# Performance work log

Hardware: AMD Instinct MI355X
Metric: run time of the kernel (lower is better)

## Reference

```python
import jax, jax.numpy as jnp
import numpy as np

V, H, NH, L, NL = 30522, 768, 12, 4, 2  # vocab, hidden, heads, layers, labels
B, S = 4, 1024
HD = H // NH  # head dim = 64


def setup_inputs() -> dict:
    key = jax.random.key(0)
    ks = jax.random.split(key, 16)
    sc = 0.02
    return {
        "input_ids": jax.random.randint(ks[0], (B, S), 0, V),
        "emb": jax.random.normal(ks[1], (V, H), jnp.float32) * sc,
        "Wq": jax.random.normal(ks[2], (L, H, H), jnp.float32) * sc,
        "bq": jnp.zeros((L, H), jnp.float32),
        "Wk": jax.random.normal(ks[3], (L, H, H), jnp.float32) * sc,
        "bk": jnp.zeros((L, H), jnp.float32),
        "Wv": jax.random.normal(ks[4], (L, H, H), jnp.float32) * sc,
        "bv": jnp.zeros((L, H), jnp.float32),
        "Wi": jax.random.normal(ks[5], (L, H, H), jnp.float32) * sc,
        "bi": jnp.zeros((L, H), jnp.float32),
        "Wo": jax.random.normal(ks[6], (L, H, H), jnp.float32) * sc,
        "bo": jnp.zeros((L, H), jnp.float32),
        "Wc": jax.random.normal(ks[7], (NL, H), jnp.float32) * sc,
        "bc": jnp.zeros((NL,), jnp.float32),
    }


def _encoder(x, Wq, bq, Wk, bk, Wv, bv, Wi, bi, Wo, bo):
    def layer(h, p):
        wq, bq_, wk, bk_, wv, bv_, wi, bi_, wo, bo_ = p
        def heads(y):  # [B,S,H] -> [B,NH,S,HD]
            return y.reshape(B, S, NH, HD).transpose(0, 2, 1, 3)
        q = heads(h @ wq.T + bq_)
        k = heads(h @ wk.T + bk_)
        v = heads(h @ wv.T + bv_)
        scores = jnp.einsum("bhqd,bhkd->bhqk", q, k) / jnp.sqrt(jnp.float32(HD))
        probs = jax.nn.softmax(scores, axis=-1)  # dropout is identity (eval)
        ctx = jnp.einsum("bhqk,bhkd->bhqd", probs, v)
        attn_out = ctx.transpose(0, 2, 1, 3).reshape(B, S, H)
        inter = jax.nn.relu(attn_out @ wi.T + bi_)
        out = inter @ wo.T + bo_ + attn_out  # residual adds attention output
        return out, None

    x, _ = jax.lax.scan(layer, x, (Wq, bq, Wk, bk, Wv, bv, Wi, bi, Wo, bo))
    return x


def reference(input_ids, emb, Wq, bq, Wk, bk, Wv, bv, Wi, bi, Wo, bo, Wc, bc):
    x = emb[input_ids]  # [B,S,H]
    x = _encoder(x, Wq, bq, Wk, bk, Wv, bv, Wi, bi, Wo, bo)
    pooled = x[:, 0]  # [B,H]
    logits = pooled @ Wc.T + bc  # [B,NL]
    return logits
```

## Files before the change

### kernel.cpp

```cpp
#include <hip/hip_runtime.h>
#include <hip/hip_bf16.h>
#include <math.h>

constexpr int Hdim = 768;
constexpr int NH   = 12;
constexpr int HD   = 64;
constexpr int NLAYER = 4;
constexpr int Bb   = 4;
constexpr int Ss   = 1024;
constexpr int Mm   = Bb * Ss;
constexpr int NL   = 2;
constexpr int PL   = Bb * NH * Ss;
constexpr float LOG2E = 1.44269504088896f;

typedef _Float16 f16x8 __attribute__((ext_vector_type(8)));
typedef _Float16 f16x4 __attribute__((ext_vector_type(4)));
typedef __fp16   h16x2 __attribute__((ext_vector_type(2)));
typedef float    f32x4 __attribute__((ext_vector_type(4)));

__device__ __forceinline__ f32x4 mfma32h(f16x8 a, f16x8 b, f32x4 c) {
#if __has_builtin(__builtin_amdgcn_mfma_f32_16x16x32_f16)
    return __builtin_amdgcn_mfma_f32_16x16x32_f16(a, b, c, 0, 0, 0);
#else
    asm("v_mfma_f32_16x16x32_f16 %0, %1, %2, %0" : "+v"(c) : "v"(a), "v"(b));
    return c;
#endif
}
__device__ __forceinline__ f32x4 mfma16h(f16x4 a, f16x4 b, f32x4 c) {
#if __has_builtin(__builtin_amdgcn_mfma_f32_16x16x16f16)
    return __builtin_amdgcn_mfma_f32_16x16x16f16(a, b, c, 0, 0, 0);
#else
    asm("v_mfma_f32_16x16x16_f16 %0, %1, %2, %0" : "+v"(c) : "v"(a), "v"(b));
    return c;
#endif
}

__device__ __forceinline__ void gload16(const void* g, void* l) {
    __builtin_amdgcn_global_load_lds(
        (const __attribute__((address_space(1))) unsigned int*)g,
        (__attribute__((address_space(3))) unsigned int*)l, 16, 0, 0);
}

__global__ void prep_kernel(const int* __restrict__ ids,
                            const float* __restrict__ emb,
                            float* __restrict__ x32, _Float16* __restrict__ xh,
                            const float* __restrict__ Wq, const float* __restrict__ Wk,
                            const float* __restrict__ Wv, const float* __restrict__ Wi,
                            const float* __restrict__ Wo,
                            _Float16* __restrict__ w16) {
    if (blockIdx.x < 3072) {
        int gidx = blockIdx.x * 256 + threadIdx.x;
        int row = gidx / 192, t = gidx - row * 192;
        int id = ids[row];
        float4 v = ((const float4*)(emb + (size_t)id * Hdim))[t];
        ((float4*)(x32 + (size_t)row * Hdim))[t] = v;
        f16x4 h;
        h[0] = (_Float16)v.x; h[1] = (_Float16)v.y;
        h[2] = (_Float16)v.z; h[3] = (_Float16)v.w;
        *(f16x4*)(xh + (size_t)row * Hdim + t * 4) = h;
    } else {
        int i = (blockIdx.x - 3072) * 256 + threadIdx.x;
        int l = i / (5 * 147456);
        int rem = i - l * (5 * 147456);
        int which = rem / 147456;
        int j = rem - which * 147456;
        const float* src = (which == 0 ? Wq : which == 1 ? Wk : which == 2 ? Wv
                          : which == 3 ? Wi : Wo) + (size_t)l * 589824;
        float4 v = ((const float4*)src)[j];
        f16x4 h;
        h[0] = (_Float16)v.x; h[1] = (_Float16)v.y;
        h[2] = (_Float16)v.z; h[3] = (_Float16)v.w;
        *(f16x4*)(w16 + ((size_t)l * 5 + which) * 589824 + (size_t)j * 4) = h;
    }
}

template<int BM>
__global__ __launch_bounds__(256) void gemm_f16(
    const _Float16* __restrict__ Xh, const _Float16* __restrict__ Wh,
    const float* __restrict__ b0, const float* __restrict__ b1,
    const float* __restrict__ b2,
    const float* __restrict__ resid32,
    _Float16* __restrict__ Yh, float* __restrict__ Y32,
    int relu, size_t outSeg, float qscale, int gm)
{
    constexpr int ABASE = BM * 64;
    constexpr int NFR   = (BM == 64) ? 4 : 2;
    __shared__ _Float16 lds[ABASE + 8192];

    const int tid = threadIdx.x;
    const int lane = tid & 63, w = tid >> 6;
    const int l15 = lane & 15, g = lane >> 4;

    const int nwg = gridDim.x;
    const int cpx = nwg >> 3;
    const int bid = blockIdx.x;
    const int x   = (bid & 7) * cpx + (bid >> 3);
    const int m0  = (x % gm) * BM;
    const int n0  = (x / gm) * 128;

    const int srow = lane >> 3;
    const int sswz = 8 * ((lane & 7) ^ srow);
    const _Float16* pA;
    _Float16* lA;
    if constexpr (BM == 64) {
        pA = Xh + (size_t)(m0 + w*16 + srow) * Hdim + sswz;
        lA = &lds[0] + w * 1024;
    } else {
        pA = Xh + (size_t)(m0 + w*8 + srow) * Hdim + sswz;
        lA = &lds[0] + w * 512;
    }
    const _Float16* pB = Wh + (size_t)(n0 + w*32 + srow) * Hdim + sswz;
    _Float16* lB = &lds[ABASE] + w * 2048;

    f32x4 acc[2][NFR];
    #pragma unroll
    for (int m = 0; m < 2; ++m)
        #pragma unroll
        for (int n = 0; n < NFR; ++n) acc[m][n] = (f32x4){0.f, 0.f, 0.f, 0.f};

    const int fsw = l15 & 7;

    for (int k0 = 0; k0 < Hdim; k0 += 64) {
        __syncthreads();
        if constexpr (BM == 64) {
            gload16(pA + k0,          lA);
            gload16(pA + k0 + 8*Hdim, lA + 512);
        } else {
            gload16(pA + k0, lA);
        }
        #pragma unroll
        for (int j = 0; j < 4; ++j)
            gload16(pB + k0 + j*8*Hdim, lB + j*512);
        __syncthreads();

        #pragma unroll
        for (int ks = 0; ks < 2; ++ks) {
            const int so = 8 * ((ks*4 + g) ^ fsw);
            f16x8 af[2], bf[NFR];
            #pragma unroll
            for (int m = 0; m < 2; ++m) {
                const int ar = (BM == 64) ? ((w >> 1)*32 + m*16 + l15)
                                          : (m*16 + l15);
                af[m] = *(const f16x8*)&lds[ar * 64 + so];
            }
            #pragma unroll
            for (int n = 0; n < NFR; ++n) {
                const int br = (BM == 64) ? ((w & 1)*64 + n*16 + l15)
                                          : (w*32 + n*16 + l15);
                bf[n] = *(const f16x8*)&lds[ABASE + br * 64 + so];
            }
            #pragma unroll
            for (int m = 0; m < 2; ++m)
                #pragma unroll
                for (int n = 0; n < NFR; ++n)
                    acc[m][n] = mfma32h(af[m], bf[n], acc[m][n]);
        }
    }

    const int rb = (BM == 64) ? (m0 + (w >> 1)*32 + g*4) : (m0 + g*4);
    #pragma unroll
    for (int n = 0; n < NFR; ++n) {
        const int col = (BM == 64) ? (n0 + (w & 1)*64 + n*16 + l15)
                                   : (n0 + w*32 + n*16 + l15);
        const int seg = col / Hdim;
        const int lc  = col - seg * Hdim;
        const float bias = (seg == 0 ? b0 : seg == 1 ? b1 : b2)[lc];
        #pragma unroll
        for (int m = 0; m < 2; ++m) {
            #pragma unroll
            for (int r = 0; r < 4; ++r) {
                const size_t idx = (size_t)seg * outSeg + (size_t)(rb + m*16 + r) * Hdim + lc;
                float v = acc[m][n][r] + bias;
                if (seg == 0) v *= qscale;
                if (relu) v = v > 0.f ? v : 0.f;
                if (resid32) v += resid32[idx];
                Yh[idx] = (_Float16)v;
                if (Y32) Y32[idx] = v;
            }
        }
    }
}

__global__ __launch_bounds__(256, 4) void attn_mfma(
    const _Float16* __restrict__ Qh, const _Float16* __restrict__ Kh,
    const _Float16* __restrict__ Vh,
    float* __restrict__ Op0, float* __restrict__ Op1,
    float* __restrict__ Mp, float* __restrict__ Lp)
{
    __shared__ _Float16 sm[17408];

    const int tid  = threadIdx.x;
    const int lane = tid & 63, wid = tid >> 6;
    const int l15  = lane & 15, g = lane >> 4;
    const int qtile = blockIdx.x >> 1, part = blockIdx.x & 1;
    const int h = blockIdx.y, b = blockIdx.z;

    const size_t rowbase = (size_t)b * Ss;
    const int    colbase = h * HD;
    const int    q0 = qtile * 128 + wid * 32;
    const int    kv0 = part * 512;

    f16x8 qf[2][2];
    #pragma unroll
    for (int nf = 0; nf < 2; ++nf) {
        const size_t r = (rowbase + q0 + nf * 16 + l15) * Hdim + colbase;
        #pragma unroll
        for (int ks = 0; ks < 2; ++ks)
            qf[nf][ks] = *(const f16x8*)(Qh + r + ks * 32 + g * 8);
    }

    f32x4 accO[4][2];
    #pragma unroll
    for (int mf = 0; mf < 4; ++mf)
        #pragma unroll
        for (int nf = 0; nf < 2; ++nf) accO[mf][nf] = (f32x4){0.f, 0.f, 0.f, 0.f};
    float mrun[2] = {-1e30f, -1e30f}, lsum[2] = {0.f, 0.f};

    const int s8 = lane >> 3;
    const int kswz = 8 * ((lane & 7) ^ s8);
    const _Float16* gK = Kh + (rowbase + kv0 + wid*16 + s8) * Hdim + colbase + kswz;

    const int kx = lane ^ (wid << 4);
    const _Float16* gV = Vh + (rowbase + kv0 + lane) * Hdim + colbase + wid * 16;
    uint4 vr[2];

    const int fsw = l15 & 7;

    gload16(gK,          &sm[0] + wid*1024);
    gload16(gK + 8*Hdim, &sm[0] + wid*1024 + 512);
    #pragma unroll
    for (int u = 0; u < 2; ++u) vr[u] = *(const uint4*)(gV + u * 8);
    #pragma unroll
    for (int u = 0; u < 2; ++u) {
        const _Float16* hs = (const _Float16*)&vr[u];
        #pragma unroll
        for (int j = 0; j < 8; ++j)
            sm[8192 + (wid*16 + u*8 + j) * 72 + kx] = hs[j];
    }
    __syncthreads();

    for (int t = 0; t < 8; ++t) {
        const int cur = t & 1;
        const int kb = cur * 4096;
        const int vb = 8192 + cur * 4608;
        if (t < 7) {
            const int nkb = (cur ^ 1) * 4096;
            const size_t ko = (size_t)((t + 1) * 64) * Hdim;
            gload16(gK + ko,          &sm[nkb] + wid*1024);
            gload16(gK + ko + 8*Hdim, &sm[nkb] + wid*1024 + 512);
            #pragma unroll
            for (int u = 0; u < 2; ++u)
                vr[u] = *(const uint4*)(gV + ko + u * 8);
        }

        f32x4 sc[4][2];
        #pragma unroll
        for (int m = 0; m < 4; ++m)
            #pragma unroll
            for (int nf = 0; nf < 2; ++nf) sc[m][nf] = (f32x4){0.f, 0.f, 0.f, 0.f};
        __builtin_amdgcn_s_setprio(1);
        #pragma unroll
        for (int ks = 0; ks < 2; ++ks) {
            const int so = 8 * ((ks*4 + g) ^ fsw);
            #pragma unroll
            for (int m = 0; m < 4; ++m) {
                f16x8 kh_ = *(const f16x8*)&sm[kb + (m * 16 + l15) * 64 + so];
                #pragma unroll
                for (int nf = 0; nf < 2; ++nf)
                    sc[m][nf] = mfma32h(kh_, qf[nf][ks], sc[m][nf]);
            }
        }
        __builtin_amdgcn_s_setprio(0);

        f16x4 pb[4][2];
        #pragma unroll
        for (int nf = 0; nf < 2; ++nf) {
            float tl = -1e30f;
            #pragma unroll
            for (int m = 0; m < 4; ++m)
                #pragma unroll
                for (int r = 0; r < 4; ++r) tl = fmaxf(tl, sc[m][nf][r]);
            if (__any(tl > mrun[nf] + 11.5416f)) {
                float tmax = fmaxf(tl, __shfl_xor(tl, 16));
                tmax = fmaxf(tmax, __shfl_xor(tmax, 32));
                const float mnew = fmaxf(mrun[nf], tmax);
                const float corr = __builtin_amdgcn_exp2f(mrun[nf] - mnew);
                mrun[nf] = mnew;
                lsum[nf] *= corr;
                #pragma unroll
                for (int mf = 0; mf < 4; ++mf) {
                    accO[mf][nf][0] *= corr; accO[mf][nf][1] *= corr;
                    accO[mf][nf][2] *= corr; accO[mf][nf][3] *= corr;
                }
            }
            float ps = 0.f;
            #pragma unroll
            for (int m = 0; m < 4; ++m)
                #pragma unroll
                for (int r = 0; r < 4; ++r) {
                    const float p = __builtin_amdgcn_exp2f(sc[m][nf][r] - mrun[nf]);
                    sc[m][nf][r] = p;
                    ps += p;
                }
            lsum[nf] += ps;
            #pragma unroll
            for (int kt = 0; kt < 4; ++kt) {
                union { h16x2 h2[2]; f16x4 v; } u;
                u.h2[0] = __builtin_amdgcn_cvt_pkrtz(sc[kt][nf][0], sc[kt][nf][1]);
                u.h2[1] = __builtin_amdgcn_cvt_pkrtz(sc[kt][nf][2], sc[kt][nf][3]);
                pb[kt][nf] = u.v;
            }
        }

        if (t < 7) {
            const int nvb = 8192 + (cur ^ 1) * 4608;
            #pragma unroll
            for (int u = 0; u < 2; ++u) {
                const _Float16* hs = (const _Float16*)&vr[u];
                #pragma unroll
                for (int j = 0; j < 8; ++j)
                    sm[nvb + (wid*16 + u*8 + j) * 72 + kx] = hs[j];
            }
        }

        __builtin_amdgcn_s_setprio(1);
        #pragma unroll
        for (int kt = 0; kt < 4; ++kt)
            #pragma unroll
            for (int mf = 0; mf < 4; ++mf) {
                const int voff = vb + (mf * 16 + l15) * 72 + ((kt ^ mf) * 16 + g * 4);
                f16x4 vh_ = *(const f16x4*)&sm[voff];
                #pragma unroll
                for (int nf = 0; nf < 2; ++nf)
                    accO[mf][nf] = mfma16h(vh_, pb[kt][nf], accO[mf][nf]);
            }
        __builtin_amdgcn_s_setprio(0);

        __syncthreads();
    }

    #pragma unroll
    for (int nf = 0; nf < 2; ++nf) {
        lsum[nf] += __shfl_xor(lsum[nf], 16);
        lsum[nf] += __shfl_xor(lsum[nf], 32);
    }
    float* ot = (float*)sm + wid * 2176;
    #pragma unroll
    for (int nf = 0; nf < 2; ++nf) {
        #pragma unroll
        for (int mf = 0; mf < 4; ++mf)
            #pragma unroll
            for (int r = 0; r < 4; ++r)
                ot[(nf * 16 + l15) * 68 + mf * 16 + g * 4 + r] = accO[mf][nf][r];
    }
    if (g == 0) {
        #pragma unroll
        for (int nf = 0; nf < 2; ++nf) {
            const size_t idx = (size_t)part * PL +
                (((size_t)b * NH + h) * Ss + q0 + nf * 16 + l15);
            Mp[idx] = mrun[nf];
            Lp[idx] = lsum[nf];
        }
    }
    __syncthreads();
    float* Op = part ? Op1 : Op0;
    const int orow = lane >> 1, oc = (lane & 1) * 32;
    const size_t pbase = (((size_t)b * NH + h) * Ss + q0 + orow) * 64 + oc;
    #pragma unroll
    for (int i = 0; i < 8; ++i)
        *(float4*)(Op + pbase + i * 4) = *(float4*)&ot[orow * 68 + oc + i * 4];
}

__global__ void merge_kernel(const float* __restrict__ Op0, const float* __restrict__ Op1,
                             const float* __restrict__ Mp, const float* __restrict__ Lp,
                             _Float16* __restrict__ a16, float* __restrict__ a32) {
    const int id = blockIdx.x * 256 + threadIdx.x;
    const int idx = id >> 2, dseg = id & 3;
    const int b = idx / (NH * Ss);
    const int rem = idx - b * NH * Ss;
    const int h = rem / Ss, q = rem - h * Ss;
    const float m0 = Mp[idx], m1 = Mp[PL + idx];
    const float l0 = Lp[idx], l1 = Lp[PL + idx];
    const float M  = fmaxf(m0, m1);
    const float e0 = __builtin_amdgcn_exp2f(m0 - M);
    const float e1 = __builtin_amdgcn_exp2f(m1 - M);
    const float inv = 1.f / (l0 * e0 + l1 * e1);
    const size_t pb = (size_t)idx * 64 + dseg * 16;
    const size_t ga = ((size_t)(b * Ss + q)) * Hdim + h * 64 + dseg * 16;
    #pragma unroll
    for (int i = 0; i < 4; ++i) {
        float4 a = *(const float4*)(Op0 + pb + i * 4);
        float4 c = *(const float4*)(Op1 + pb + i * 4);
        float4 o;
        o.x = (a.x * e0 + c.x * e1) * inv;
        o.y = (a.y * e0 + c.y * e1) * inv;
        o.z = (a.z * e0 + c.z * e1) * inv;
        o.w = (a.w * e0 + c.w * e1) * inv;
        *(float4*)(a32 + ga + i * 4) = o;
        f16x4 hh;
        hh[0] = (_Float16)o.x; hh[1] = (_Float16)o.y;
        hh[2] = (_Float16)o.z; hh[3] = (_Float16)o.w;
        *(f16x4*)(a16 + ga + i * 4) = hh;
    }
}

__global__ void cls_kernel(const float* __restrict__ x32,
                           const float* __restrict__ Wc,
                           const float* __restrict__ bc,
                           float* __restrict__ out) {
    const int b = blockIdx.x >> 1;
    const int n = blockIdx.x & 1;
    const int t = threadIdx.x;
    const float* px = x32 + (size_t)b * Ss * Hdim;
    const float* pw = Wc + (size_t)n * Hdim;
    float partial = 0.f;
    for (int k = t; k < Hdim; k += 256) partial = fmaf(px[k], pw[k], partial);
    __shared__ float red[256];
    red[t] = partial;
    __syncthreads();
    for (int off = 128; off > 0; off >>= 1) {
        if (t < off) red[t] += red[t + off];
        __syncthreads();
    }
    if (t == 0) out[blockIdx.x] = red[0] + bc[n];
}

extern "C" void kernel_launch(void* const* d_in, const int* in_sizes, int n_in,
                              void* d_out, int out_size, void* d_ws, size_t ws_size,
                              hipStream_t stream) {
    const int*   ids = (const int*)d_in[0];
    const float* emb = (const float*)d_in[1];
    const float* Wq  = (const float*)d_in[2];
    const float* bq  = (const float*)d_in[3];
    const float* Wk  = (const float*)d_in[4];
    const float* bk  = (const float*)d_in[5];
    const float* Wv  = (const float*)d_in[6];
    const float* bv  = (const float*)d_in[7];
    const float* Wi  = (const float*)d_in[8];
    const float* bi  = (const float*)d_in[9];
    const float* Wo  = (const float*)d_in[10];
    const float* bo  = (const float*)d_in[11];
    const float* Wc  = (const float*)d_in[12];
    const float* bc  = (const float*)d_in[13];
    float* out = (float*)d_out;

    const size_t F  = (size_t)Mm * Hdim;
    const size_t WS = (size_t)Hdim * Hdim;

    float*    x32 = (float*)d_ws;
    _Float16* xh  = (_Float16*)(x32 + F);
    _Float16* qkv = xh + F;
    _Float16* a16 = qkv + 3 * F;
    _Float16* i16 = a16 + F;
    _Float16* w16 = i16 + F;
    float*    a32 = (float*)(w16 + 20 * WS);
    float*    Op0 = a32 + F;
    float*    Op1 = Op0 + F;
    float*    Mp  = Op1 + F;
    float*    Lp  = Mp + 2 * PL;

    prep_kernel<<<14592, 256, 0, stream>>>(ids, emb, x32, xh, Wq, Wk, Wv, Wi, Wo, w16);

    for (int l = 0; l < NLAYER; ++l) {
        _Float16* wl = w16 + (size_t)l * 5 * WS;
        gemm_f16<64><<<1152, 256, 0, stream>>>(
            xh, wl, bq + l*Hdim, bk + l*Hdim, bv + l*Hdim,
            nullptr, qkv, nullptr, 0, F, 0.125f * LOG2E, 64);
        attn_mfma<<<dim3(16, NH, Bb), 256, 0, stream>>>(
            qkv, qkv + F, qkv + 2*F, Op0, Op1, Mp, Lp);
        merge_kernel<<<PL * 4 / 256, 256, 0, stream>>>(Op0, Op1, Mp, Lp, a16, a32);
        gemm_f16<32><<<768, 256, 0, stream>>>(
            a16, wl + 3*WS, bi + l*Hdim, bi + l*Hdim, bi + l*Hdim,
            nullptr, i16, nullptr, 1, 0, 1.f, 128);
        gemm_f16<32><<<768, 256, 0, stream>>>(
            i16, wl + 4*WS, bo + l*Hdim, bo + l*Hdim, bo + l*Hdim,
            a32, xh, x32, 0, 0, 1.f, 128);
    }

    cls_kernel<<<Bb * NL, 256, 0, stream>>>(x32, Wc, bc, out);
}
```

Measured before the change: 412.6 us.

## Fuse split-attention merge into the Wi GEMM A-load and the Wo GEMM residual epilogue

Drops the separate merge kernel. The intermediate GEMM now combines the two attention partials (Op0/Op1 with their max and sum stats) while loading its A tile, converting to fp16 straight into LDS. The output GEMM recomputes the merged attention value in its epilogue to add as the residual. The fp32 x32 copy is written only on the last layer, which removes the a16/a32 buffers and their traffic, at the cost of redundant stat loads, exp2 and divides in both GEMMs and a loss of async A-tile loads.

```diff
diff --git a/kernel.cpp b/kernel.cpp
--- a/kernel.cpp
+++ b/kernel.cpp
@@ -74,12 +74,13 @@
     }
 }
 
-template<int BM>
+template<int BM, int MODE>
 __global__ __launch_bounds__(256) void gemm_f16(
     const _Float16* __restrict__ Xh, const _Float16* __restrict__ Wh,
     const float* __restrict__ b0, const float* __restrict__ b1,
     const float* __restrict__ b2,
-    const float* __restrict__ resid32,
+    const float* __restrict__ Op0, const float* __restrict__ Op1,
+    const float* __restrict__ Mp, const float* __restrict__ Lp,
     _Float16* __restrict__ Yh, float* __restrict__ Y32,
     int relu, size_t outSeg, float qscale, int gm)
 {
@@ -100,18 +101,21 @@
 
     const int srow = lane >> 3;
     const int sswz = 8 * ((lane & 7) ^ srow);
-    const _Float16* pA;
-    _Float16* lA;
-    if constexpr (BM == 64) {
-        pA = Xh + (size_t)(m0 + w*16 + srow) * Hdim + sswz;
-        lA = &lds[0] + w * 1024;
-    } else {
-        pA = Xh + (size_t)(m0 + w*8 + srow) * Hdim + sswz;
-        lA = &lds[0] + w * 512;
-    }
     const _Float16* pB = Wh + (size_t)(n0 + w*32 + srow) * Hdim + sswz;
     _Float16* lB = &lds[ABASE] + w * 2048;
 
+    const _Float16* pA = nullptr;
+    _Float16* lA = nullptr;
+    if constexpr (MODE != 1) {
+        if constexpr (BM == 64) {
+            pA = Xh + (size_t)(m0 + w*16 + srow) * Hdim + sswz;
+            lA = &lds[0] + w * 1024;
+        } else {
+            pA = Xh + (size_t)(m0 + w*8 + srow) * Hdim + sswz;
+            lA = &lds[0] + w * 512;
+        }
+    }
+
     f32x4 acc[2][NFR];
     #pragma unroll
     for (int m = 0; m < 2; ++m)
@@ -122,11 +126,39 @@
 
     for (int k0 = 0; k0 < Hdim; k0 += 64) {
         __syncthreads();
-        if constexpr (BM == 64) {
-            gload16(pA + k0,          lA);
-            gload16(pA + k0 + 8*Hdim, lA + 512);
+        if constexpr (MODE == 1) {
+            const int r  = tid >> 3;
+            const int sg = tid & 7;
+            const int m  = m0 + r;
+            const size_t idxr = ((size_t)(m >> 10) * NH + (k0 >> 6)) * Ss + (m & 1023);
+            const float m0_ = Mp[idxr], m1_ = Mp[PL + idxr];
+            const float l0_ = Lp[idxr], l1_ = Lp[PL + idxr];
+            const float Mx  = fmaxf(m0_, m1_);
+            const float e0  = __builtin_amdgcn_exp2f(m0_ - Mx);
+            const float e1  = __builtin_amdgcn_exp2f(m1_ - Mx);
+            const float inv = 1.f / (l0_ * e0 + l1_ * e1);
+            const size_t pb2 = idxr * 64 + sg * 8;
+            float4 a0 = *(const float4*)(Op0 + pb2);
+            float4 a1 = *(const float4*)(Op0 + pb2 + 4);
+            float4 c0 = *(const float4*)(Op1 + pb2);
+            float4 c1 = *(const float4*)(Op1 + pb2 + 4);
+            union { h16x2 h2[4]; f16x8 v; } u;
+            u.h2[0] = __builtin_amdgcn_cvt_pkrtz((a0.x*e0 + c0.x*e1)*inv,
+                                                 (a0.y*e0 + c0.y*e1)*inv);
+            u.h2[1] = __builtin_amdgcn_cvt_pkrtz((a0.z*e0 + c0.z*e1)*inv,
+                                                 (a0.w*e0 + c0.w*e1)*inv);
+            u.h2[2] = __builtin_amdgcn_cvt_pkrtz((a1.x*e0 + c1.x*e1)*inv,
+                                                 (a1.y*e0 + c1.y*e1)*inv);
+            u.h2[3] = __builtin_amdgcn_cvt_pkrtz((a1.z*e0 + c1.z*e1)*inv,
+                                                 (a1.w*e0 + c1.w*e1)*inv);
+            *(f16x8*)&lds[r * 64 + 8 * (sg ^ (r & 7))] = u.v;
         } else {
-            gload16(pA + k0, lA);
+            if constexpr (BM == 64) {
+                gload16(pA + k0,          lA);
+                gload16(pA + k0 + 8*Hdim, lA + 512);
+            } else {
+                gload16(pA + k0, lA);
+            }
         }
         #pragma unroll
         for (int j = 0; j < 4; ++j)
@@ -169,11 +201,23 @@
         for (int m = 0; m < 2; ++m) {
             #pragma unroll
             for (int r = 0; r < 4; ++r) {
-                const size_t idx = (size_t)seg * outSeg + (size_t)(rb + m*16 + r) * Hdim + lc;
+                const int row = rb + m*16 + r;
+                const size_t idx = (size_t)seg * outSeg + (size_t)row * Hdim + lc;
                 float v = acc[m][n][r] + bias;
                 if (seg == 0) v *= qscale;
                 if (relu) v = v > 0.f ? v : 0.f;
-                if (resid32) v += resid32[idx];
+                if constexpr (MODE == 2) {
+                    const size_t idxr = ((size_t)(row >> 10) * NH + (lc >> 6)) * Ss
+                                        + (row & 1023);
+                    const float m0_ = Mp[idxr], m1_ = Mp[PL + idxr];
+                    const float l0_ = Lp[idxr], l1_ = Lp[PL + idxr];
+                    const float Mx  = fmaxf(m0_, m1_);
+                    const float e0  = __builtin_amdgcn_exp2f(m0_ - Mx);
+                    const float e1  = __builtin_amdgcn_exp2f(m1_ - Mx);
+                    const float inv = 1.f / (l0_ * e0 + l1_ * e1);
+                    const size_t po = idxr * 64 + (lc & 63);
+                    v += (Op0[po] * e0 + Op1[po] * e1) * inv;
+                }
                 Yh[idx] = (_Float16)v;
                 if (Y32) Y32[idx] = v;
             }
@@ -369,39 +413,6 @@
     #pragma unroll
     for (int i = 0; i < 8; ++i)
         *(float4*)(Op + pbase + i * 4) = *(float4*)&ot[orow * 68 + oc + i * 4];
-}
-
-__global__ void merge_kernel(const float* __restrict__ Op0, const float* __restrict__ Op1,
-                             const float* __restrict__ Mp, const float* __restrict__ Lp,
-                             _Float16* __restrict__ a16, float* __restrict__ a32) {
-    const int id = blockIdx.x * 256 + threadIdx.x;
-    const int idx = id >> 2, dseg = id & 3;
-    const int b = idx / (NH * Ss);
-    const int rem = idx - b * NH * Ss;
-    const int h = rem / Ss, q = rem - h * Ss;
-    const float m0 = Mp[idx], m1 = Mp[PL + idx];
-    const float l0 = Lp[idx], l1 = Lp[PL + idx];
-    const float M  = fmaxf(m0, m1);
-    const float e0 = __builtin_amdgcn_exp2f(m0 - M);
-    const float e1 = __builtin_amdgcn_exp2f(m1 - M);
-    const float inv = 1.f / (l0 * e0 + l1 * e1);
-    const size_t pb = (size_t)idx * 64 + dseg * 16;
-    const size_t ga = ((size_t)(b * Ss + q)) * Hdim + h * 64 + dseg * 16;
-    #pragma unroll
-    for (int i = 0; i < 4; ++i) {
-        float4 a = *(const float4*)(Op0 + pb + i * 4);
-        float4 c = *(const float4*)(Op1 + pb + i * 4);
-        float4 o;
-        o.x = (a.x * e0 + c.x * e1) * inv;
-        o.y = (a.y * e0 + c.y * e1) * inv;
-        o.z = (a.z * e0 + c.z * e1) * inv;
-        o.w = (a.w * e0 + c.w * e1) * inv;
-        *(float4*)(a32 + ga + i * 4) = o;
-        f16x4 hh;
-        hh[0] = (_Float16)o.x; hh[1] = (_Float16)o.y;
-        hh[2] = (_Float16)o.z; hh[3] = (_Float16)o.w;
-        *(f16x4*)(a16 + ga + i * 4) = hh;
-    }
 }
 
 __global__ void cls_kernel(const float* __restrict__ x32,
@@ -450,11 +461,9 @@
     float*    x32 = (float*)d_ws;
     _Float16* xh  = (_Float16*)(x32 + F);
     _Float16* qkv = xh + F;
-    _Float16* a16 = qkv + 3 * F;
-    _Float16* i16 = a16 + F;
+    _Float16* i16 = qkv + 3 * F;
     _Float16* w16 = i16 + F;
-    float*    a32 = (float*)(w16 + 20 * WS);
-    float*    Op0 = a32 + F;
+    float*    Op0 = (float*)(w16 + 20 * WS);
     float*    Op1 = Op0 + F;
     float*    Mp  = Op1 + F;
     float*    Lp  = Mp + 2 * PL;
@@ -463,18 +472,20 @@
 
     for (int l = 0; l < NLAYER; ++l) {
         _Float16* wl = w16 + (size_t)l * 5 * WS;
-        gemm_f16<64><<<1152, 256, 0, stream>>>(
+        gemm_f16<64, 0><<<1152, 256, 0, stream>>>(
             xh, wl, bq + l*Hdim, bk + l*Hdim, bv + l*Hdim,
-            nullptr, qkv, nullptr, 0, F, 0.125f * LOG2E, 64);
+            nullptr, nullptr, nullptr, nullptr,
+            qkv, nullptr, 0, F, 0.125f * LOG2E, 64);
         attn_mfma<<<dim3(16, NH, Bb), 256, 0, stream>>>(
             qkv, qkv + F, qkv + 2*F, Op0, Op1, Mp, Lp);
-        merge_kernel<<<PL * 4 / 256, 256, 0, stream>>>(Op0, Op1, Mp, Lp, a16, a32);
-        gemm_f16<32><<<768, 256, 0, stream>>>(
-            a16, wl + 3*WS, bi + l*Hdim, bi + l*Hdim, bi + l*Hdim,
-            nullptr, i16, nullptr, 1, 0, 1.f, 128);
-        gemm_f16<32><<<768, 256, 0, stream>>>(
+        gemm_f16<32, 1><<<768, 256, 0, stream>>>(
+            nullptr, wl + 3*WS, bi + l*Hdim, bi + l*Hdim, bi + l*Hdim,
+            Op0, Op1, Mp, Lp,
+            i16, nullptr, 1, 0, 1.f, 128);
+        gemm_f16<32, 2><<<768, 256, 0, stream>>>(
             i16, wl + 4*WS, bo + l*Hdim, bo + l*Hdim, bo + l*Hdim,
-            a32, xh, x32, 0, 0, 1.f, 128);
+            Op0, Op1, Mp, Lp,
+            xh, (l == NLAYER - 1) ? x32 : nullptr, 0, 0, 1.f, 128);
     }
 
     cls_kernel<<<Bb * NL, 256, 0, stream>>>(x32, Wc, bc, out);
```

After: 427.5 us. 3.6% more time.

## Store attention partials in fp16 and write fp32 output only for pooled rows

Applied to the files above, without the earlier changes.

The split-KV attention partial outputs are now stored as fp16 instead of fp32, which halves the traffic between the attention and merge kernels. The merge kernel folds the normalisation into per-part scales and uses 8-wide fp16 loads. The fp32 hidden-state copy is no longer written by the embedding prep. The final layer's output GEMM writes fp32 only for the CLS rows that the classifier reads, since the residual uses a32, not x32. The cost is some precision loss in the unnormalised partial outputs stored in fp16.

```diff
diff --git a/kernel.cpp b/kernel.cpp
--- a/kernel.cpp
+++ b/kernel.cpp
@@ -43,7 +43,7 @@
 
 __global__ void prep_kernel(const int* __restrict__ ids,
                             const float* __restrict__ emb,
-                            float* __restrict__ x32, _Float16* __restrict__ xh,
+                            _Float16* __restrict__ xh,
                             const float* __restrict__ Wq, const float* __restrict__ Wk,
                             const float* __restrict__ Wv, const float* __restrict__ Wi,
                             const float* __restrict__ Wo,
@@ -53,7 +53,6 @@
         int row = gidx / 192, t = gidx - row * 192;
         int id = ids[row];
         float4 v = ((const float4*)(emb + (size_t)id * Hdim))[t];
-        ((float4*)(x32 + (size_t)row * Hdim))[t] = v;
         f16x4 h;
         h[0] = (_Float16)v.x; h[1] = (_Float16)v.y;
         h[2] = (_Float16)v.z; h[3] = (_Float16)v.w;
@@ -169,13 +168,14 @@
         for (int m = 0; m < 2; ++m) {
             #pragma unroll
             for (int r = 0; r < 4; ++r) {
-                const size_t idx = (size_t)seg * outSeg + (size_t)(rb + m*16 + r) * Hdim + lc;
+                const int row = rb + m*16 + r;
+                const size_t idx = (size_t)seg * outSeg + (size_t)row * Hdim + lc;
                 float v = acc[m][n][r] + bias;
                 if (seg == 0) v *= qscale;
                 if (relu) v = v > 0.f ? v : 0.f;
                 if (resid32) v += resid32[idx];
                 Yh[idx] = (_Float16)v;
-                if (Y32) Y32[idx] = v;
+                if (Y32 && (row & 1023) == 0) Y32[idx] = v;
             }
         }
     }
@@ -184,7 +184,7 @@
 __global__ __launch_bounds__(256, 4) void attn_mfma(
     const _Float16* __restrict__ Qh, const _Float16* __restrict__ Kh,
     const _Float16* __restrict__ Vh,
-    float* __restrict__ Op0, float* __restrict__ Op1,
+    _Float16* __restrict__ Op0, _Float16* __restrict__ Op1,
     float* __restrict__ Mp, float* __restrict__ Lp)
 {
     __shared__ _Float16 sm[17408];
@@ -344,15 +344,17 @@
         lsum[nf] += __shfl_xor(lsum[nf], 16);
         lsum[nf] += __shfl_xor(lsum[nf], 32);
     }
-    float* ot = (float*)sm + wid * 2176;
-    #pragma unroll
-    for (int nf = 0; nf < 2; ++nf) {
-        #pragma unroll
-        for (int mf = 0; mf < 4; ++mf)
-            #pragma unroll
-            for (int r = 0; r < 4; ++r)
-                ot[(nf * 16 + l15) * 68 + mf * 16 + g * 4 + r] = accO[mf][nf][r];
-    }
+    __syncthreads();
+    _Float16* ot16 = (_Float16*)sm + wid * 2304;
+    #pragma unroll
+    for (int nf = 0; nf < 2; ++nf)
+        #pragma unroll
+        for (int mf = 0; mf < 4; ++mf) {
+            union { h16x2 h2[2]; f16x4 v; } u;
+            u.h2[0] = __builtin_amdgcn_cvt_pkrtz(accO[mf][nf][0], accO[mf][nf][1]);
+            u.h2[1] = __builtin_amdgcn_cvt_pkrtz(accO[mf][nf][2], accO[mf][nf][3]);
+            *(f16x4*)&ot16[(nf * 16 + l15) * 72 + mf * 16 + g * 4] = u.v;
+        }
     if (g == 0) {
         #pragma unroll
         for (int nf = 0; nf < 2; ++nf) {
@@ -363,15 +365,16 @@
         }
     }
     __syncthreads();
-    float* Op = part ? Op1 : Op0;
+    _Float16* Op = part ? Op1 : Op0;
     const int orow = lane >> 1, oc = (lane & 1) * 32;
     const size_t pbase = (((size_t)b * NH + h) * Ss + q0 + orow) * 64 + oc;
     #pragma unroll
-    for (int i = 0; i < 8; ++i)
-        *(float4*)(Op + pbase + i * 4) = *(float4*)&ot[orow * 68 + oc + i * 4];
-}
-
-__global__ void merge_kernel(const float* __restrict__ Op0, const float* __restrict__ Op1,
+    for (int i = 0; i < 4; ++i)
+        *(f16x8*)(Op + pbase + i * 8) = *(const f16x8*)&ot16[orow * 72 + oc + i * 8];
+}
+
+__global__ void merge_kernel(const _Float16* __restrict__ Op0,
+                             const _Float16* __restrict__ Op1,
                              const float* __restrict__ Mp, const float* __restrict__ Lp,
                              _Float16* __restrict__ a16, float* __restrict__ a32) {
     const int id = blockIdx.x * 256 + threadIdx.x;
@@ -385,22 +388,26 @@
     const float e0 = __builtin_amdgcn_exp2f(m0 - M);
     const float e1 = __builtin_amdgcn_exp2f(m1 - M);
     const float inv = 1.f / (l0 * e0 + l1 * e1);
+    const float s0 = e0 * inv, s1 = e1 * inv;
     const size_t pb = (size_t)idx * 64 + dseg * 16;
     const size_t ga = ((size_t)(b * Ss + q)) * Hdim + h * 64 + dseg * 16;
     #pragma unroll
-    for (int i = 0; i < 4; ++i) {
-        float4 a = *(const float4*)(Op0 + pb + i * 4);
-        float4 c = *(const float4*)(Op1 + pb + i * 4);
-        float4 o;
-        o.x = (a.x * e0 + c.x * e1) * inv;
-        o.y = (a.y * e0 + c.y * e1) * inv;
-        o.z = (a.z * e0 + c.z * e1) * inv;
-        o.w = (a.w * e0 + c.w * e1) * inv;
-        *(float4*)(a32 + ga + i * 4) = o;
-        f16x4 hh;
-        hh[0] = (_Float16)o.x; hh[1] = (_Float16)o.y;
-        hh[2] = (_Float16)o.z; hh[3] = (_Float16)o.w;
-        *(f16x4*)(a16 + ga + i * 4) = hh;
+    for (int i = 0; i < 2; ++i) {
+        f16x8 a = *(const f16x8*)(Op0 + pb + i * 8);
+        f16x8 c = *(const f16x8*)(Op1 + pb + i * 8);
+        f16x8 ho;
+        float ov[8];
+        #pragma unroll
+        for (int j = 0; j < 8; ++j) {
+            const float v = (float)a[j] * s0 + (float)c[j] * s1;
+            ov[j] = v;
+            ho[j] = (_Float16)v;
+        }
+        *(f16x8*)(a16 + ga + i * 8) = ho;
+        float4 q0 = make_float4(ov[0], ov[1], ov[2], ov[3]);
+        float4 q1 = make_float4(ov[4], ov[5], ov[6], ov[7]);
+        *(float4*)(a32 + ga + i * 8)     = q0;
+        *(float4*)(a32 + ga + i * 8 + 4) = q1;
     }
 }
 
@@ -453,13 +460,13 @@
     _Float16* a16 = qkv + 3 * F;
     _Float16* i16 = a16 + F;
     _Float16* w16 = i16 + F;
-    float*    a32 = (float*)(w16 + 20 * WS);
-    float*    Op0 = a32 + F;
-    float*    Op1 = Op0 + F;
-    float*    Mp  = Op1 + F;
+    _Float16* Op0 = w16 + 20 * WS;
+    _Float16* Op1 = Op0 + F;
+    float*    a32 = (float*)(Op1 + F);
+    float*    Mp  = a32 + F;
     float*    Lp  = Mp + 2 * PL;
 
-    prep_kernel<<<14592, 256, 0, stream>>>(ids, emb, x32, xh, Wq, Wk, Wv, Wi, Wo, w16);
+    prep_kernel<<<14592, 256, 0, stream>>>(ids, emb, xh, Wq, Wk, Wv, Wi, Wo, w16);
 
     for (int l = 0; l < NLAYER; ++l) {
         _Float16* wl = w16 + (size_t)l * 5 * WS;
@@ -474,7 +481,7 @@
             nullptr, i16, nullptr, 1, 0, 1.f, 128);
         gemm_f16<32><<<768, 256, 0, stream>>>(
             i16, wl + 4*WS, bo + l*Hdim, bo + l*Hdim, bo + l*Hdim,
-            a32, xh, x32, 0, 0, 1.f, 128);
+            a32, xh, (l == NLAYER - 1) ? x32 : nullptr, 0, 0, 1.f, 128);
     }
 
     cls_kernel<<<Bb * NL, 256, 0, stream>>>(x32, Wc, bc, out);
```

After: 382.2 us, median of 2. 1.08x faster.
